# Kernel tuning notes

Measured on AMD Instinct MI355X. Metric: run time of the kernel, lower is better.

Reference implementation:

```python
import jax, jax.numpy as jnp
import numpy as np

BLOCK = 128  # block_size in the original module


def weight_dequant(weight, scale):
    # weight: [O, I] fp8 values (simulated float32); scale: [O//BLOCK, I//BLOCK] fp32
    O, I = weight.shape
    w = weight.reshape(O // BLOCK, BLOCK, I // BLOCK, BLOCK)
    w = w * scale[:, None, :, None]
    return w.reshape(O, I)


def setup_inputs() -> dict:
    key = jax.random.key(0)
    k1, k2, k3, k4 = jax.random.split(key, 4)
    B, S, IN, OUT = 2, 2048, 4096, 16384
    x = jax.random.normal(k1, (B, S, IN), dtype=jnp.float32)
    weight = jax.random.normal(k2, (OUT, IN), dtype=jnp.float32)
    scale = jax.random.uniform(k3, (OUT // BLOCK, IN // BLOCK), dtype=jnp.float32, minval=0.01, maxval=0.05)
    bias = jax.random.normal(k4, (OUT,), dtype=jnp.float32)
    return {"x": x, "weight": weight, "scale": scale, "bias": bias}


def reference(x, weight, scale, bias):
    # bf16 gemm_impl path: block-wise dequant of fp8 weight, then F.linear(x, W) + bias
    w = weight_dequant(weight, scale)          # [O, I]
    out = jnp.einsum('bsi,oi->bso', x, w)      # x @ W^T
    return out + bias
```

## Files before the change

kernel.cpp:

```cpp
#include <hip/hip_runtime.h>
#include <hip/hip_bf16.h>

#define M_DIM 4096
#define N_DIM 16384
#define K_DIM 4096

typedef __bf16 bf16x8 __attribute__((ext_vector_type(8)));
typedef float f32x4 __attribute__((ext_vector_type(4)));

__device__ __forceinline__ void gload16(const void* g, void* l) {
    __builtin_amdgcn_global_load_lds((__attribute__((address_space(1))) void*)g,
                                     (__attribute__((address_space(3))) void*)l, 16, 0, 0);
}

__global__ __launch_bounds__(256) void cvt_x_kernel(const float* __restrict__ x,
                                                    __hip_bfloat16* __restrict__ out,
                                                    int ngroups) {
    int i = blockIdx.x * blockDim.x + threadIdx.x;
    int stride = gridDim.x * blockDim.x;
    for (; i < ngroups; i += stride) {
        const float4* p = (const float4*)(x + (size_t)i * 8);
        float4 v0 = p[0];
        float4 v1 = p[1];
        bf16x8 r;
        r[0] = (__bf16)v0.x; r[1] = (__bf16)v0.y; r[2] = (__bf16)v0.z; r[3] = (__bf16)v0.w;
        r[4] = (__bf16)v1.x; r[5] = (__bf16)v1.y; r[6] = (__bf16)v1.z; r[7] = (__bf16)v1.w;
        *(bf16x8*)(out + (size_t)i * 8) = r;
    }
}

__global__ __launch_bounds__(256) void dequant_w_kernel(const float* __restrict__ w,
                                                        const float* __restrict__ scale,
                                                        __hip_bfloat16* __restrict__ out) {
    const int ngroups = N_DIM * (K_DIM / 8);
    int i = blockIdx.x * blockDim.x + threadIdx.x;
    int stride = gridDim.x * blockDim.x;
    for (; i < ngroups; i += stride) {
        int row = i >> 9;
        int cg  = i & 511;
        float s = scale[(row >> 7) * (K_DIM / 128) + (cg >> 4)];
        const float4* p = (const float4*)(w + (size_t)i * 8);
        float4 v0 = p[0];
        float4 v1 = p[1];
        bf16x8 r;
        r[0] = (__bf16)(v0.x * s); r[1] = (__bf16)(v0.y * s);
        r[2] = (__bf16)(v0.z * s); r[3] = (__bf16)(v0.w * s);
        r[4] = (__bf16)(v1.x * s); r[5] = (__bf16)(v1.y * s);
        r[6] = (__bf16)(v1.z * s); r[7] = (__bf16)(v1.w * s);
        *(bf16x8*)(out + (size_t)i * 8) = r;
    }
}

__global__ __launch_bounds__(512, 2)
void gemm_bf16_kernel(const __hip_bfloat16* __restrict__ A,
                      const __hip_bfloat16* __restrict__ Bw,
                      const float* __restrict__ bias,
                      float* __restrict__ C) {
    constexpr int Mtiles = M_DIM / 256;
    constexpr int Ntiles = N_DIM / 256;
    constexpr int nwg = Mtiles * Ntiles;

    int bid = blockIdx.x;
    int swz = (bid & 7) * (nwg >> 3) + (bid >> 3);
    int bm = swz % Mtiles;
    int bn = swz / Mtiles;

    __shared__ __align__(16) __hip_bfloat16 sA[2][256 * 64];
    __shared__ __align__(16) __hip_bfloat16 sB[2][256 * 64];

    const int t = threadIdx.x;
    const int l = t & 63;
    const int w = t >> 6;
    const int wm = w >> 2;
    const int wn = w & 3;

    const int lr = l & 15;
    const int lk = l >> 4;
    const int rx = (lr & 7) << 3;

    const int srow = w * 8 + (l >> 3);
    const int scol = ((l & 7) ^ (l >> 3)) << 3;

    const size_t K = K_DIM;
    const __hip_bfloat16* aB = A  + (size_t)(bm * 256) * K + scol;
    const __hip_bfloat16* bB = Bw + (size_t)(bn * 256) * K + scol;

    f32x4 acc[8][4] = {};

    const int c0 = (lk * 8) ^ rx;
    const int c1 = (32 + lk * 8) ^ rx;
    const int arow = (wm * 128 + lr) * 64;
    const int brow = (wn * 64 + lr) * 64;

    char* A0b = (char*)&sA[0][0] + w * 1024;
    char* B0b = (char*)&sB[0][0] + w * 1024;
    char* A1b = (char*)&sA[1][0] + w * 1024;
    char* B1b = (char*)&sB[1][0] + w * 1024;

#define SH(lbase, gptr)                                                         \
    do {                                                                        \
        gload16((gptr) + (size_t)srow * K, (lbase));                            \
        gload16((gptr) + (size_t)(64 + srow) * K, (lbase) + 8192);              \
    } while (0)

#define RD_A(dst, off)                                                          \
    _Pragma("unroll")                                                           \
    for (int mi = 0; mi < 4; ++mi) {                                            \
        dst[mi][0] = *(const bf16x8*)(pa_ + arow + (off) + mi * 1024 + c0);     \
        dst[mi][1] = *(const bf16x8*)(pa_ + arow + (off) + mi * 1024 + c1);     \
    }

#define RD_B(dst, off)                                                          \
    _Pragma("unroll")                                                           \
    for (int ni = 0; ni < 2; ++ni) {                                            \
        dst[ni][0] = *(const bf16x8*)(pb_ + brow + (off) + ni * 1024 + c0);     \
        dst[ni][1] = *(const bf16x8*)(pb_ + brow + (off) + ni * 1024 + c1);     \
    }

#define MM(mo, no, af, bf)                                                      \
    do {                                                                        \
        __builtin_amdgcn_s_setprio(1);                                          \
        _Pragma("unroll")                                                       \
        for (int s = 0; s < 2; ++s)                                             \
            _Pragma("unroll")                                                   \
            for (int mi = 0; mi < 4; ++mi)                                      \
                _Pragma("unroll")                                               \
                for (int ni = 0; ni < 2; ++ni)                                  \
                    acc[(mo) + mi][(no) + ni] =                                 \
                        __builtin_amdgcn_mfma_f32_16x16x32_bf16(                \
                            af[mi][s], bf[ni][s], acc[(mo) + mi][(no) + ni],    \
                            0, 0, 0);                                           \
        __builtin_amdgcn_s_setprio(0);                                          \
    } while (0)

#define BAR()  __builtin_amdgcn_s_barrier()
#define SBAR() __builtin_amdgcn_sched_barrier(0)
#define LGKM0() do { asm volatile("s_waitcnt lgkmcnt(0)" ::: "memory"); SBAR(); } while (0)

    bf16x8 a03[4][2], a47[4][2], b01[2][2], b23[2][2];

    SH(A0b, aB);  SH(A0b + 16384, aB + (size_t)128 * K);
    SH(B0b, bB);  SH(B0b + 16384, bB + (size_t)128 * K);
    SH(B1b, bB + 64);  SH(B1b + 16384, bB + 64 + (size_t)128 * K);
    asm volatile("s_waitcnt vmcnt(4)" ::: "memory");
    SBAR();
    BAR();

    #pragma unroll 1
    for (int p = 0; p < 32; ++p) {
        const bool last = (p == 31);
        const __hip_bfloat16* gAu  = aB + (size_t)(2 * p + 1) * 64;
        const __hip_bfloat16* gAt2 = aB + (size_t)(2 * p + 2) * 64;
        const __hip_bfloat16* gBt2 = bB + (size_t)(2 * p + 2) * 64;
        const __hip_bfloat16* gBt3 = bB + (size_t)(2 * p + 3) * 64;
        const __hip_bfloat16* pa_;
        const __hip_bfloat16* pb_;

        pa_ = &sA[0][0]; pb_ = &sB[0][0];
        RD_A(a03, 0); RD_B(b01, 0);
        SH(A1b, gAu);
        SBAR();
        asm volatile("s_waitcnt lgkmcnt(8)" ::: "memory");
        BAR();
        LGKM0();
        MM(0, 0, a03, b01);
        SBAR(); BAR();
        RD_B(b23, 2048);
        SH(A1b + 16384, gAu + (size_t)128 * K);
        SBAR(); BAR();
        LGKM0();
        MM(0, 2, a03, b23);
        SBAR(); BAR();
        RD_A(a47, 4096);
        if (!last) SH(B0b, gBt2);
        SBAR(); BAR();
        LGKM0();
        MM(4, 0, a47, b01);
        SBAR(); BAR();
        if (!last) {
            SH(B0b + 16384, gBt2 + (size_t)128 * K);
            asm volatile("s_waitcnt vmcnt(4)" ::: "memory");
        } else {
            asm volatile("s_waitcnt vmcnt(0)" ::: "memory");
        }
        SBAR(); BAR();
        MM(4, 2, a47, b23);
        SBAR(); BAR();

        pa_ = &sA[1][0]; pb_ = &sB[1][0];
        RD_A(a03, 0); RD_B(b01, 0);
        if (!last) SH(A0b, gAt2);
        SBAR();
        asm volatile("s_waitcnt lgkmcnt(8)" ::: "memory");
        BAR();
        LGKM0();
        MM(0, 0, a03, b01);
        SBAR(); BAR();
        RD_B(b23, 2048);
        if (!last) SH(A0b + 16384, gAt2 + (size_t)128 * K);
        SBAR(); BAR();
        LGKM0();
        MM(0, 2, a03, b23);
        SBAR(); BAR();
        RD_A(a47, 4096);
        if (!last) SH(B1b, gBt3);
        SBAR(); BAR();
        LGKM0();
        MM(4, 0, a47, b01);
        SBAR(); BAR();
        if (!last) {
            SH(B1b + 16384, gBt3 + (size_t)128 * K);
            asm volatile("s_waitcnt vmcnt(4)" ::: "memory");
        }
        SBAR(); BAR();
        MM(4, 2, a47, b23);
        SBAR();
        if (!last) BAR();
    }
#undef SH
#undef RD_A
#undef RD_B
#undef MM
#undef BAR
#undef SBAR
#undef LGKM0

    const int crow0 = bm * 256 + wm * 128;
    const int ccol0 = bn * 256 + wn * 64;
    #pragma unroll
    for (int ni = 0; ni < 4; ++ni) {
        int col = ccol0 + ni * 16 + lr;
        float bv = bias[col];
        #pragma unroll
        for (int mi = 0; mi < 8; ++mi) {
            int rbase = crow0 + mi * 16 + lk * 4;
            #pragma unroll
            for (int j = 0; j < 4; ++j) {
                C[(size_t)(rbase + j) * N_DIM + col] = acc[mi][ni][j] + bv;
            }
        }
    }
}

__global__ __launch_bounds__(256)
void gemm_fallback(const float* __restrict__ X, const float* __restrict__ W,
                   const float* __restrict__ scale, const float* __restrict__ bias,
                   float* __restrict__ C) {
    int bm = blockIdx.x % (M_DIM / 64);
    int bn = blockIdx.x / (M_DIM / 64);
    __shared__ float sA[64][33];
    __shared__ float sB[64][33];
    int t = threadIdx.x;
    int tx = t & 15, ty = t >> 4;
    float acc[4][4] = {};
    for (int kt = 0; kt < K_DIM / 32; ++kt) {
        float s = scale[(bn >> 1) * (K_DIM / 128) + (kt >> 2)];
        #pragma unroll
        for (int i = 0; i < 8; ++i) {
            int idx = t + i * 256;
            int r = idx >> 5, c = idx & 31;
            sA[r][c] = X[(size_t)(bm * 64 + r) * K_DIM + kt * 32 + c];
            sB[r][c] = W[(size_t)(bn * 64 + r) * K_DIM + kt * 32 + c] * s;
        }
        __syncthreads();
        #pragma unroll
        for (int k = 0; k < 32; ++k) {
            float a[4], b[4];
            #pragma unroll
            for (int i = 0; i < 4; ++i) a[i] = sA[ty * 4 + i][k];
            #pragma unroll
            for (int j = 0; j < 4; ++j) b[j] = sB[tx * 4 + j][k];
            #pragma unroll
            for (int i = 0; i < 4; ++i)
                #pragma unroll
                for (int j = 0; j < 4; ++j) acc[i][j] += a[i] * b[j];
        }
        __syncthreads();
    }
    #pragma unroll
    for (int i = 0; i < 4; ++i)
        #pragma unroll
        for (int j = 0; j < 4; ++j) {
            int row = bm * 64 + ty * 4 + i;
            int col = bn * 64 + tx * 4 + j;
            C[(size_t)row * N_DIM + col] = acc[i][j] + bias[col];
        }
}

extern "C" void kernel_launch(void* const* d_in, const int* in_sizes, int n_in,
                              void* d_out, int out_size, void* d_ws, size_t ws_size,
                              hipStream_t stream) {
    const float* x     = (const float*)d_in[0];
    const float* wgt   = (const float*)d_in[1];
    const float* scale = (const float*)d_in[2];
    const float* bias  = (const float*)d_in[3];
    float* out = (float*)d_out;

    const size_t need = ((size_t)M_DIM * K_DIM + (size_t)N_DIM * K_DIM) * sizeof(__hip_bfloat16);
    if (ws_size >= need) {
        __hip_bfloat16* xbf = (__hip_bfloat16*)d_ws;
        __hip_bfloat16* wbf = xbf + (size_t)M_DIM * K_DIM;
        cvt_x_kernel<<<2048, 256, 0, stream>>>(x, xbf, M_DIM * K_DIM / 8);
        dequant_w_kernel<<<4096, 256, 0, stream>>>(wgt, scale, wbf);
        gemm_bf16_kernel<<<(M_DIM / 256) * (N_DIM / 256), 512, 0, stream>>>(xbf, wbf, bias, out);
    } else {
        gemm_fallback<<<(M_DIM / 64) * (N_DIM / 64), 256, 0, stream>>>(x, wgt, scale, bias, out);
    }
}
```

Measured before the change: 710.8 us.

## Software-pipeline LDS fragment reads one MFMA phase ahead with fewer barriers

Restructures the main GEMM loop so the LDS fragment reads for the next MFMA phase are issued before the current phase's MFMAs. Partial lgkmcnt/vmcnt waits replace full drains, barriers drop from two per phase to one, and the last iteration is peeled into an epilogue. The goal is to hide LDS read latency and global-to-LDS load latency behind matrix work. In exchange it needs careful counter accounting, where a miscount could give races, and it holds more fragment registers live at once.

```diff
diff --git a/kernel.cpp b/kernel.cpp
--- a/kernel.cpp
+++ b/kernel.cpp
@@ -96,26 +96,46 @@
     char* B0b = (char*)&sB[0][0] + w * 1024;
     char* A1b = (char*)&sA[1][0] + w * 1024;
     char* B1b = (char*)&sB[1][0] + w * 1024;
-
-#define SH(lbase, gptr)                                                         \
+    const __hip_bfloat16* pa0 = &sA[0][0];
+    const __hip_bfloat16* pb0 = &sB[0][0];
+    const __hip_bfloat16* pa1 = &sA[1][0];
+    const __hip_bfloat16* pb1 = &sB[1][0];
+
+    bf16x8 a03[4][2], a47[4][2], b01[2][2], b23[2][2];
+
+#define SH(lb, gp)                                                              \
     do {                                                                        \
-        gload16((gptr) + (size_t)srow * K, (lbase));                            \
-        gload16((gptr) + (size_t)(64 + srow) * K, (lbase) + 8192);              \
+        gload16((gp) + (size_t)srow * K, (lb));                                 \
+        gload16((gp) + (size_t)(64 + srow) * K, (lb) + 8192);                   \
     } while (0)
 
-#define RD_A(dst, off)                                                          \
-    _Pragma("unroll")                                                           \
-    for (int mi = 0; mi < 4; ++mi) {                                            \
-        dst[mi][0] = *(const bf16x8*)(pa_ + arow + (off) + mi * 1024 + c0);     \
-        dst[mi][1] = *(const bf16x8*)(pa_ + arow + (off) + mi * 1024 + c1);     \
-    }
-
-#define RD_B(dst, off)                                                          \
-    _Pragma("unroll")                                                           \
-    for (int ni = 0; ni < 2; ++ni) {                                            \
-        dst[ni][0] = *(const bf16x8*)(pb_ + brow + (off) + ni * 1024 + c0);     \
-        dst[ni][1] = *(const bf16x8*)(pb_ + brow + (off) + ni * 1024 + c1);     \
-    }
+#define RD_A03(pa_)                                                             \
+    { _Pragma("unroll")                                                         \
+      for (int mi = 0; mi < 4; ++mi) {                                          \
+          a03[mi][0] = *(const bf16x8*)((pa_) + arow + mi * 1024 + c0);         \
+          a03[mi][1] = *(const bf16x8*)((pa_) + arow + mi * 1024 + c1);         \
+      } }
+
+#define RD_A47(pa_)                                                             \
+    { _Pragma("unroll")                                                         \
+      for (int mi = 0; mi < 4; ++mi) {                                          \
+          a47[mi][0] = *(const bf16x8*)((pa_) + arow + 4096 + mi * 1024 + c0);  \
+          a47[mi][1] = *(const bf16x8*)((pa_) + arow + 4096 + mi * 1024 + c1);  \
+      } }
+
+#define RD_B01(pb_)                                                             \
+    { _Pragma("unroll")                                                         \
+      for (int ni = 0; ni < 2; ++ni) {                                          \
+          b01[ni][0] = *(const bf16x8*)((pb_) + brow + ni * 1024 + c0);         \
+          b01[ni][1] = *(const bf16x8*)((pb_) + brow + ni * 1024 + c1);         \
+      } }
+
+#define RD_B23(pb_)                                                             \
+    { _Pragma("unroll")                                                         \
+      for (int ni = 0; ni < 2; ++ni) {                                          \
+          b23[ni][0] = *(const bf16x8*)((pb_) + brow + 2048 + ni * 1024 + c0);  \
+          b23[ni][1] = *(const bf16x8*)((pb_) + brow + 2048 + ni * 1024 + c1);  \
+      } }
 
 #define MM(mo, no, af, bf)                                                      \
     do {                                                                        \
@@ -131,99 +151,113 @@
                             af[mi][s], bf[ni][s], acc[(mo) + mi][(no) + ni],    \
                             0, 0, 0);                                           \
         __builtin_amdgcn_s_setprio(0);                                          \
+        __builtin_amdgcn_sched_barrier(0);                                      \
     } while (0)
 
-#define BAR()  __builtin_amdgcn_s_barrier()
 #define SBAR() __builtin_amdgcn_sched_barrier(0)
-#define LGKM0() do { asm volatile("s_waitcnt lgkmcnt(0)" ::: "memory"); SBAR(); } while (0)
-
-    bf16x8 a03[4][2], a47[4][2], b01[2][2], b23[2][2];
-
-    SH(A0b, aB);  SH(A0b + 16384, aB + (size_t)128 * K);
-    SH(B0b, bB);  SH(B0b + 16384, bB + (size_t)128 * K);
-    SH(B1b, bB + 64);  SH(B1b + 16384, bB + 64 + (size_t)128 * K);
-    asm volatile("s_waitcnt vmcnt(4)" ::: "memory");
+#define WAITL(n) do { asm volatile("s_waitcnt lgkmcnt(" #n ")" ::: "memory"); SBAR(); } while (0)
+#define WAITV(n) do { asm volatile("s_waitcnt vmcnt(" #n ")" ::: "memory"); SBAR(); } while (0)
+#define BARS() do { __builtin_amdgcn_s_barrier(); SBAR(); } while (0)
+
+    SH(A0b, aB);             SH(A0b + 16384, aB + (size_t)128 * K);
+    SH(B0b, bB);             SH(B0b + 16384, bB + (size_t)128 * K);
+    SH(B1b, bB + 64);
+    SH(A1b, aB + 64);        SH(A1b + 16384, aB + 64 + (size_t)128 * K);
+    WAITV(6);
+    BARS();
+    RD_A03(pa0);
+    RD_B01(pb0);
     SBAR();
-    BAR();
 
     #pragma unroll 1
-    for (int p = 0; p < 32; ++p) {
-        const bool last = (p == 31);
-        const __hip_bfloat16* gAu  = aB + (size_t)(2 * p + 1) * 64;
+    for (int p = 0; p < 31; ++p) {
+        const __hip_bfloat16* gBu  = bB + (size_t)(2 * p + 1) * 64;
         const __hip_bfloat16* gAt2 = aB + (size_t)(2 * p + 2) * 64;
         const __hip_bfloat16* gBt2 = bB + (size_t)(2 * p + 2) * 64;
-        const __hip_bfloat16* gBt3 = bB + (size_t)(2 * p + 3) * 64;
-        const __hip_bfloat16* pa_;
-        const __hip_bfloat16* pb_;
-
-        pa_ = &sA[0][0]; pb_ = &sB[0][0];
-        RD_A(a03, 0); RD_B(b01, 0);
-        SH(A1b, gAu);
-        SBAR();
-        asm volatile("s_waitcnt lgkmcnt(8)" ::: "memory");
-        BAR();
-        LGKM0();
+        const __hip_bfloat16* gAu2 = aB + (size_t)(2 * p + 3) * 64;
+        const __hip_bfloat16* gBu2 = bB + (size_t)(2 * p + 3) * 64;
+
+        SH(B1b + 16384, gBu + (size_t)128 * K);
+        RD_B23(pb0);
+        WAITL(4); BARS();
         MM(0, 0, a03, b01);
-        SBAR(); BAR();
-        RD_B(b23, 2048);
-        SH(A1b + 16384, gAu + (size_t)128 * K);
-        SBAR(); BAR();
-        LGKM0();
+
+        RD_A47(pa0);
+        WAITL(8); BARS();
         MM(0, 2, a03, b23);
-        SBAR(); BAR();
-        RD_A(a47, 4096);
-        if (!last) SH(B0b, gBt2);
-        SBAR(); BAR();
-        LGKM0();
+
+        WAITV(2);
+        SH(B0b, gBt2);
+        RD_A03(pa1);
+        WAITL(8); BARS();
         MM(4, 0, a47, b01);
-        SBAR(); BAR();
-        if (!last) {
-            SH(B0b + 16384, gBt2 + (size_t)128 * K);
-            asm volatile("s_waitcnt vmcnt(4)" ::: "memory");
-        } else {
-            asm volatile("s_waitcnt vmcnt(0)" ::: "memory");
-        }
-        SBAR(); BAR();
+
+        WAITV(2);
+        SH(A0b, gAt2);       SH(A0b + 16384, gAt2 + (size_t)128 * K);
+        RD_B01(pb1);
+        WAITL(12); BARS();
         MM(4, 2, a47, b23);
-        SBAR(); BAR();
-
-        pa_ = &sA[1][0]; pb_ = &sB[1][0];
-        RD_A(a03, 0); RD_B(b01, 0);
-        if (!last) SH(A0b, gAt2);
-        SBAR();
-        asm volatile("s_waitcnt lgkmcnt(8)" ::: "memory");
-        BAR();
-        LGKM0();
+
+        SH(B0b + 16384, gBt2 + (size_t)128 * K);
+        RD_B23(pb1);
+        WAITL(4); BARS();
         MM(0, 0, a03, b01);
-        SBAR(); BAR();
-        RD_B(b23, 2048);
-        if (!last) SH(A0b + 16384, gAt2 + (size_t)128 * K);
-        SBAR(); BAR();
-        LGKM0();
+
+        RD_A47(pa1);
+        WAITL(8); BARS();
         MM(0, 2, a03, b23);
-        SBAR(); BAR();
-        RD_A(a47, 4096);
-        if (!last) SH(B1b, gBt3);
-        SBAR(); BAR();
-        LGKM0();
+
+        WAITV(2);
+        SH(B1b, gBu2);
+        RD_A03(pa0);
+        WAITL(8); BARS();
         MM(4, 0, a47, b01);
-        SBAR(); BAR();
-        if (!last) {
-            SH(B1b + 16384, gBt3 + (size_t)128 * K);
-            asm volatile("s_waitcnt vmcnt(4)" ::: "memory");
-        }
-        SBAR(); BAR();
+
+        WAITV(2);
+        SH(A1b, gAu2);       SH(A1b + 16384, gAu2 + (size_t)128 * K);
+        RD_B01(pb0);
+        WAITL(12); BARS();
         MM(4, 2, a47, b23);
-        SBAR();
-        if (!last) BAR();
+    }
+
+    {
+        const __hip_bfloat16* gBu = bB + (size_t)63 * 64;
+        SH(B1b + 16384, gBu + (size_t)128 * K);
+        RD_B23(pb0);
+        WAITL(4); BARS();
+        MM(0, 0, a03, b01);
+        RD_A47(pa0);
+        WAITL(8); BARS();
+        MM(0, 2, a03, b23);
+        WAITV(2);
+        RD_A03(pa1);
+        WAITL(8); BARS();
+        MM(4, 0, a47, b01);
+        WAITV(0);
+        RD_B01(pb1);
+        WAITL(12); BARS();
+        MM(4, 2, a47, b23);
+        RD_B23(pb1);
+        WAITL(4); BARS();
+        MM(0, 0, a03, b01);
+        RD_A47(pa1);
+        WAITL(8); BARS();
+        MM(0, 2, a03, b23);
+        WAITL(0); BARS();
+        MM(4, 0, a47, b01);
+        WAITL(0); BARS();
+        MM(4, 2, a47, b23);
     }
 #undef SH
-#undef RD_A
-#undef RD_B
+#undef RD_A03
+#undef RD_A47
+#undef RD_B01
+#undef RD_B23
 #undef MM
-#undef BAR
 #undef SBAR
-#undef LGKM0
+#undef WAITL
+#undef WAITV
+#undef BARS
 
     const int crow0 = bm * 256 + wm * 128;
     const int ccol0 = bn * 256 + wn * 64;
```

Result: slower. 895.3 us (+26.0%).
